# Optimization experiments

Measured on AMD Instinct MI355X. Metric: run time of the kernel, lower is better.

The kernel has to match this reference:

```python
import jax, jax.numpy as jnp
import numpy as np

WS = 8            # window_size
SHIFT = WS // 2   # cyclic shift
NHEADS = 6
EPS = 1e-5


def _rel_pos_index(ws):
    coords = np.stack(np.meshgrid(np.arange(ws), np.arange(ws), indexing='ij'))  # [2,ws,ws]
    flat = coords.reshape(2, -1)                       # [2,N]
    rel = flat[:, :, None] - flat[:, None, :]          # [2,N,N]
    rel = rel.transpose(1, 2, 0).copy()
    rel[:, :, 0] += ws - 1
    rel[:, :, 1] += ws - 1
    rel[:, :, 0] *= 2 * ws - 1
    return rel.sum(-1)                                 # [N,N] indices into bias table


def _attn_mask(H, W, ws, shift):
    # standard Swin boundary mask for the shifted configuration
    img = np.zeros((H, W))
    cnt = 0
    for hs in (slice(0, -ws), slice(-ws, -shift), slice(-shift, None)):
        for wsl in (slice(0, -ws), slice(-ws, -shift), slice(-shift, None)):
            img[hs, wsl] = cnt
            cnt += 1
    mw = img.reshape(H // ws, ws, W // ws, ws).transpose(0, 2, 1, 3).reshape(-1, ws * ws)
    m = mw[:, None, :] - mw[:, :, None]
    return np.where(m != 0, -100.0, 0.0).astype(np.float32)  # [nW, N, N]


def instance_norm(x):
    # InstanceNorm over spatial dims, no affine (torch default)
    m = x.mean(axis=(2, 3), keepdims=True)
    v = x.var(axis=(2, 3), keepdims=True)
    return (x - m) * jax.lax.rsqrt(v + EPS)


def setup_inputs() -> dict:
    key = jax.random.key(0)
    ks = jax.random.split(key, 8)
    B, C, H, W, E = 4, 192, 256, 256, 128
    s = 0.02
    return {
        'x': jax.random.normal(ks[0], (B, C, H, W), jnp.float32),
        'cond': jax.random.normal(ks[1], (B, E), jnp.float32),
        'qkv_w': jax.random.normal(ks[2], (3 * C, C), jnp.float32) * s,
        'qkv_b': jnp.zeros((3 * C,), jnp.float32),
        'proj_w': jax.random.normal(ks[3], (C, C), jnp.float32) * s,
        'proj_b': jnp.zeros((C,), jnp.float32),
        'rel_bias': jax.random.normal(ks[4], ((2 * WS - 1) ** 2, NHEADS), jnp.float32) * s,
        'film_w': jax.random.normal(ks[5], (2 * C, E), jnp.float32) * s,
        'film_b': jnp.zeros((2 * C,), jnp.float32),
    }


def shifted_window_attention(xn, qkv_w, qkv_b, proj_w, proj_b, rel_bias):
    B, C, H, W = xn.shape
    h, ws, shift = NHEADS, WS, SHIFT
    d = C // h
    N = ws * ws
    nW = (H // ws) * (W // ws)
    scale = d ** -0.5

    xs = jnp.transpose(xn, (0, 2, 3, 1))                         # BHWC
    xs = jnp.roll(xs, (-shift, -shift), axis=(1, 2))             # cyclic shift
    win = xs.reshape(B, H // ws, ws, W // ws, ws, C)
    win = win.transpose(0, 1, 3, 2, 4, 5).reshape(B * nW, N, C)  # window partition

    qkv = win @ qkv_w.T + qkv_b                                  # [Bn, N, 3C]
    q, k, v = [t.reshape(B * nW, N, h, d).transpose(0, 2, 1, 3)
               for t in jnp.split(qkv, 3, axis=-1)]              # [Bn, h, N, d]

    attn = jnp.einsum('bhnd,bhmd->bhnm', q, k) * scale           # [Bn, h, N, N]
    bias = rel_bias[_rel_pos_index(ws)].transpose(2, 0, 1)       # [h, N, N]
    attn = attn + bias[None]
    mask = jnp.asarray(_attn_mask(H, W, ws, shift))              # [nW, N, N]
    attn = attn.reshape(B, nW, h, N, N) + mask[None, :, None]
    attn = jax.nn.softmax(attn, axis=-1).reshape(B * nW, h, N, N)

    out = jnp.einsum('bhnm,bhmd->bhnd', attn, v)                 # [Bn, h, N, d]
    out = out.transpose(0, 2, 1, 3).reshape(B * nW, N, C)
    out = out @ proj_w.T + proj_b

    out = out.reshape(B, H // ws, W // ws, ws, ws, C)
    out = out.transpose(0, 1, 3, 2, 4, 5).reshape(B, H, W, C)    # window merge
    out = jnp.roll(out, (shift, shift), axis=(1, 2))             # reverse shift
    return jnp.transpose(out, (0, 3, 1, 2))                      # BCHW


def reference(x, cond, qkv_w, qkv_b, proj_w, proj_b, rel_bias, film_w, film_b):
    # branch 1: x + attn(norm1(x))
    xn = instance_norm(x)
    x = x + shifted_window_attention(xn, qkv_w, qkv_b, proj_w, proj_b, rel_bias)
    # branch 2: x + FiLM(norm2(x), cond)
    x2 = instance_norm(x)
    gb = cond @ film_w.T + film_b                                # [B, 2C]
    gamma, beta = jnp.split(gb, 2, axis=-1)
    x2 = x2 * gamma[:, :, None, None] + beta[:, :, None, None]
    return x + x2
```

## Files before the change

### kernel.cpp

```cpp
#include <hip/hip_runtime.h>

#define BATCH 4
#define CH    192
#define PLANE 65536

typedef unsigned short u16;
typedef unsigned char  u8;
typedef __bf16 bf16x8_t __attribute__((ext_vector_type(8)));
typedef unsigned short u16x8 __attribute__((ext_vector_type(8)));
typedef unsigned short u16x4 __attribute__((ext_vector_type(4)));
typedef float f32x4 __attribute__((ext_vector_type(4)));

__device__ __forceinline__ u16 f2bf(float f) {
  __bf16 h = (__bf16)f;
  return __builtin_bit_cast(u16, h);
}
__device__ __forceinline__ float bf2f(u16 h) {
  unsigned u = ((unsigned)h) << 16;
  return __builtin_bit_cast(float, u);
}
__device__ __forceinline__ f32x4 mfma16(u16x8 a, u16x8 b, f32x4 c) {
  return __builtin_amdgcn_mfma_f32_16x16x32_bf16(
      __builtin_bit_cast(bf16x8_t, a), __builtin_bit_cast(bf16x8_t, b), c, 0, 0, 0);
}

__global__ void cvt_kernel(const float* __restrict__ a, const float* __restrict__ b,
                           const float* __restrict__ rb,
                           u16* __restrict__ wa, u16* __restrict__ wb, u8* __restrict__ bq) {
  const int i = blockIdx.x*256 + threadIdx.x;
  if (i < 576*192) wa[i] = f2bf(a[i]);
  if (i < 192*192) wb[i] = f2bf(b[i]);
  if (i < 1350) {
    float v = fminf(fmaxf(rintf(rb[i]*128.f) + 128.f, 0.f), 255.f);
    bq[i] = (u8)v;
  }
}

__global__ void film_prep(const float* __restrict__ cond, const float* __restrict__ fw,
                          const float* __restrict__ fb, float* __restrict__ gb) {
  const int i = blockIdx.x*256 + threadIdx.x;
  if (i >= BATCH*384) return;
  const int bb = i / 384, oc = i - bb*384;
  const float* cw = fw + oc*128;
  const float* cv = cond + bb*128;
  float s = fb[oc];
  for (int k = 0; k < 128; ++k) s += cv[k]*cw[k];
  gb[i] = s;
}

__global__ __launch_bounds__(256) void prep_kernel(
    const float* __restrict__ x, u16* __restrict__ xraw, float2* __restrict__ part1)
{
  __shared__ u16 tile[32*264];
  const int t = threadIdx.x;
  const int bid = blockIdx.x;
  const int cc = bid % 6;
  const int wh = (bid/6) % 32;
  const int b  = bid / 192;
  const int c0 = cc*32;
  const int ww = t >> 3, ax = t & 7;
  const int gx = (ww*8 + ax + 4) & 255;
  const int gxb = gx & ~3, gxr = gx & 3;
  const long wid = b*1024 + wh*32 + ww;

  const int scl = t >> 3, sseg = t & 7;
  float myS = 0.f, myQ = 0.f;

  for (int ay = 0; ay < 8; ++ay) {
    const int gy = (wh*8 + ay + 4) & 255;
    for (int it = 0; it < 8; ++it) {
      const int id = it*256 + t;
      const int cl = id >> 6;
      const int px = (id & 63) << 2;
      float4 v = *(const float4*)(x + (((long)(b*192+c0+cl)) << 16) + gy*256 + px);
      u16x4 pk;
      pk[0] = f2bf(v.x); pk[1] = f2bf(v.y); pk[2] = f2bf(v.z); pk[3] = f2bf(v.w);
      *(u16x4*)&tile[cl*264 + (px ^ ((cl&7)<<2))] = pk;
    }
    __syncthreads();
    {
      const int sw = (scl & 7) << 2;
      #pragma unroll
      for (int k = 0; k < 32; k += 4) {
        const int px = sseg*32 + k;
        u16x4 pv = *(const u16x4*)&tile[scl*264 + (px ^ sw)];
        float a0 = bf2f(pv[0]), a1 = bf2f(pv[1]), a2 = bf2f(pv[2]), a3 = bf2f(pv[3]);
        myS += a0 + a1 + a2 + a3;
        myQ += a0*a0 + a1*a1 + a2*a2 + a3*a3;
      }
    }
    u16* dst = xraw + wid*12288 + (ay*8+ax)*192 + c0;
    #pragma unroll
    for (int k = 0; k < 4; ++k) {
      u16x8 pk;
      #pragma unroll
      for (int e = 0; e < 8; ++e) {
        const int c = k*8 + e;
        pk[e] = tile[c*264 + (gxb ^ ((c&7)<<2)) + gxr];
      }
      *(u16x8*)(dst + k*8) = pk;
    }
    __syncthreads();
  }
  for (int off = 1; off < 8; off <<= 1) {
    myS += __shfl_xor(myS, off, 64);
    myQ += __shfl_xor(myQ, off, 64);
  }
  if (sseg == 0) {
    float2 pr = {myS, myQ};
    part1[((b*32 + wh)*6 + cc)*32 + scl] = pr;
  }
}

__global__ __launch_bounds__(256) void statsR_kernel(
    const float2* __restrict__ part1, float* __restrict__ st) {
  const int i = blockIdx.x*256 + threadIdx.x;
  if (i >= 768) return;
  const int b = i / 192, c = i % 192;
  const int cg = c >> 5, cl = c & 31;
  float s = 0.f, q = 0.f;
  for (int wh = 0; wh < 32; ++wh) {
    float2 v = part1[((b*32 + wh)*6 + cg)*32 + cl];
    s += v.x; q += v.y;
  }
  const float mean = s * (1.f/PLANE);
  const float var  = q * (1.f/PLANE) - mean*mean;
  st[i*2]   = mean;
  st[i*2+1] = rsqrtf(var + 1e-5f);
}

__global__ __launch_bounds__(512, 4) void attn_kernel(
    const u16* __restrict__ xn, const u16* __restrict__ wq, const u16* __restrict__ wp,
    const float* __restrict__ qkvb, const float* __restrict__ projb,
    const u8* __restrict__ bq, const float* __restrict__ st,
    u16* __restrict__ pw, float2* __restrict__ part)
{
  __shared__ __attribute__((aligned(16))) unsigned char smem[73232];
  u16*    Xs    = (u16*)smem;
  u16*    G     = (u16*)(smem + 25600);
  u16*    Vt    = (u16*)(smem + 43008);
  u16*    Pout  = (u16*)(smem + 25600);
  u8*     biasQ = (u8*)(smem + 52224);
  float2* stpNp = (float2*)(smem + 53576);
  float2* stpR  = (float2*)(smem + 55304);
  u16*    Ps    = (u16*)(smem + 56848);

  const int t    = threadIdx.x;
  const int lane = t & 63;
  const int wave = t >> 6;
  const int arow = lane & 15;
  const int kgrp = lane >> 4;

  const int bid = blockIdx.x;
  const int wid = (bid & 7) * 512 + (bid >> 3);
  const int b   = wid >> 10;
  const int wh  = (wid >> 5) & 31;
  const int ww  = wid & 31;

  for (int i = t; i < 1350; i += 512) biasQ[i] = bq[i];
  if (t < 192) {
    const float mean = st[(b*192 + t)*2];
    const float rstd = st[(b*192 + t)*2 + 1];
    float2 n = {mean, rstd};
    float2 r = {mean, 1.0f / rstd};
    stpNp[t + (t >> 3)] = n;
    stpR[t] = r;
  }
  __syncthreads();

  const u16* src = xn + (long)wid*12288;
  #pragma unroll
  for (int it = 0; it < 3; ++it) {
    const int id = it*512 + t;
    const int row = id/24, c8 = (id%24)*8;
    const int sbase = c8 + (c8 >> 3);
    u16x8 raw = *(const u16x8*)(src + id*8);
    u16x8 nrm;
    #pragma unroll
    for (int e = 0; e < 8; ++e) {
      float2 mr = stpNp[sbase + e];
      nrm[e] = f2bf((bf2f(raw[e]) - mr.x) * mr.y);
    }
    *(u16x8*)&Xs[row*200 + c8] = nrm;
  }
  __syncthreads();

  const int hh = wave >> 2;
  const int mt = wave & 3;
  const bool boundary = (wh == 31) || (ww == 31);
  u16x4 og[3][2];

  #pragma unroll
  for (int g = 0; g < 3; ++g) {
    for (int nt0 = wave; nt0 < 12; nt0 += 8) {
      f32x4 acc[4] = {{0,0,0,0},{0,0,0,0},{0,0,0,0},{0,0,0,0}};
      const int col = nt0*16 + arow;
      const int mat = col >> 6;
      const int ch  = mat*192 + g*64 + (col & 63);
      const u16* wrow = wq + ch*192 + kgrp*8;
      #pragma unroll
      for (int ks = 0; ks < 6; ++ks) {
        u16x8 bfr = *(const u16x8*)(wrow + ks*32);
        #pragma unroll
        for (int m = 0; m < 4; ++m) {
          u16x8 af = *(const u16x8*)&Xs[(m*16+arow)*200 + ks*32 + kgrp*8];
          acc[m] = mfma16(af, bfr, acc[m]);
        }
      }
      const float addb = qkvb[ch];
      if (mat == 2) {
        const int vc = col & 63;
        #pragma unroll
        for (int m = 0; m < 4; ++m) {
          u16x4 pk;
          #pragma unroll
          for (int r = 0; r < 4; ++r) pk[r] = f2bf(acc[m][r] + addb);
          *(u16x4*)&Vt[vc*72 + m*16 + kgrp*4] = pk;
        }
      } else {
        const float mult = (mat == 0) ? 0.17677669529663687f : 1.0f;
        const int gc = mat*64 + (col & 63);
        #pragma unroll
        for (int m = 0; m < 4; ++m)
          #pragma unroll
          for (int r = 0; r < 4; ++r)
            G[(m*16 + kgrp*4 + r)*136 + gc] = f2bf((acc[m][r] + addb)*mult);
      }
    }
    __syncthreads();

    const int hd = g*2 + hh;
    u16x8 qf = *(const u16x8*)&G[(mt*16+arow)*136 + hh*32 + kgrp*8];
    f32x4 sv[4];
    #pragma unroll
    for (int nt = 0; nt < 4; ++nt) {
      u16x8 kf = *(const u16x8*)&G[(nt*16+arow)*136 + 64 + hh*32 + kgrp*8];
      f32x4 z = {0,0,0,0};
      sv[nt] = mfma16(qf, kf, z);
    }

    int qj6[4];
    #pragma unroll
    for (int nt = 0; nt < 4; ++nt) {
      const int j = nt*16 + arow;
      qj6[nt] = ((j>>3)*15 + (j&7))*6;
    }
    float p[4][4];
    if (!boundary) {
      #pragma unroll
      for (int r = 0; r < 4; ++r) {
        const int i = mt*16 + kgrp*4 + r;
        const int qib = ((i>>3)*15 + (i&7) + 112)*6 + hd;
        #pragma unroll
        for (int nt = 0; nt < 4; ++nt)
          p[nt][r] = sv[nt][r] + (float)((int)biasQ[qib - qj6[nt]] - 128) * 0.0078125f;
      }
    } else {
      #pragma unroll
      for (int r = 0; r < 4; ++r) {
        const int i  = mt*16 + kgrp*4 + r;
        const int iy = i >> 3, ix = i & 7;
        const int qib = (iy*15 + ix + 112)*6 + hd;
        const int ri = ((wh==31) ? (iy<4?1:2) : 0)*3 + ((ww==31) ? (ix<4?1:2) : 0);
        #pragma unroll
        for (int nt = 0; nt < 4; ++nt) {
          const int j  = nt*16 + arow;
          const int jy = j >> 3, jx = j & 7;
          const int rj = ((wh==31) ? (jy<4?1:2) : 0)*3 + ((ww==31) ? (jx<4?1:2) : 0);
          float sc = sv[nt][r] + (float)((int)biasQ[qib - qj6[nt]] - 128) * 0.0078125f;
          if (ri != rj) sc -= 100.0f;
          p[nt][r] = sc;
        }
      }
    }
    #pragma unroll
    for (int r = 0; r < 4; ++r) {
      float sum = 0.f;
      #pragma unroll
      for (int nt = 0; nt < 4; ++nt) { p[nt][r] = __expf(p[nt][r]); sum += p[nt][r]; }
      for (int off = 1; off < 16; off <<= 1) sum += __shfl_xor(sum, off, 64);
      const float inv = 1.0f / sum;
      #pragma unroll
      for (int nt = 0; nt < 4; ++nt) p[nt][r] *= inv;
    }
    u16* myP = Ps + wave*1024;
    #pragma unroll
    for (int r = 0; r < 4; ++r) {
      const int i = kgrp*4 + r;
      #pragma unroll
      for (int nt = 0; nt < 4; ++nt) {
        const int j = nt*16 + arow;
        myP[i*64 + ((j + 8*i) & 63)] = f2bf(p[nt][r]);
      }
    }
    f32x4 oacc[2] = {{0,0,0,0},{0,0,0,0}};
    #pragma unroll
    for (int ks = 0; ks < 2; ++ks) {
      u16x8 pf = *(const u16x8*)&myP[arow*64 + ((ks*32 + kgrp*8 + 8*arow) & 63)];
      #pragma unroll
      for (int nt = 0; nt < 2; ++nt) {
        u16x8 vf = *(const u16x8*)&Vt[(hh*32 + nt*16 + arow)*72 + ks*32 + kgrp*8];
        oacc[nt] = mfma16(pf, vf, oacc[nt]);
      }
    }
    #pragma unroll
    for (int nt = 0; nt < 2; ++nt)
      #pragma unroll
      for (int r = 0; r < 4; ++r)
        og[g][nt][r] = f2bf(oacc[nt][r]);
    __syncthreads();
  }

  u16x8 rawreg[3];
  #pragma unroll
  for (int it = 0; it < 3; ++it) {
    const int id = it*512 + t;
    const int c = id >> 3, tk8 = (id & 7)*8;
    const float2 mi = stpR[c];
    u16x8 rr;
    #pragma unroll
    for (int e = 0; e < 8; ++e) {
      float nv = bf2f(Xs[(tk8 + e)*200 + c]);
      rr[e] = f2bf(nv*mi.y + mi.x);
    }
    rawreg[it] = rr;
  }
  __syncthreads();

  #pragma unroll
  for (int g = 0; g < 3; ++g)
    #pragma unroll
    for (int nt = 0; nt < 2; ++nt) {
      const int colb = g*64 + hh*32 + nt*16 + arow;
      #pragma unroll
      for (int r = 0; r < 4; ++r)
        Xs[(mt*16 + kgrp*4 + r)*200 + colb] = og[g][nt][r];
    }
  __syncthreads();

  for (int nt0 = wave; nt0 < 12; nt0 += 8) {
    const int ch = nt0*16 + arow;
    const float pb = projb[ch];
    f32x4 acc[4];
    #pragma unroll
    for (int m = 0; m < 4; ++m) { f32x4 v = {pb,pb,pb,pb}; acc[m] = v; }
    const u16* wrow = wp + ch*192 + kgrp*8;
    #pragma unroll
    for (int ks = 0; ks < 6; ++ks) {
      u16x8 bfr = *(const u16x8*)(wrow + ks*32);
      #pragma unroll
      for (int m = 0; m < 4; ++m) {
        u16x8 af = *(const u16x8*)&Xs[(m*16+arow)*200 + ks*32 + kgrp*8];
        acc[m] = mfma16(af, bfr, acc[m]);
      }
    }
    #pragma unroll
    for (int m = 0; m < 4; ++m) {
      u16x4 pk;
      #pragma unroll
      for (int r = 0; r < 4; ++r) pk[r] = f2bf(acc[m][r]);
      *(u16x4*)&Pout[ch*72 + m*16 + kgrp*4] = pk;
    }
  }
  __syncthreads();

  u16* dstw = pw + (long)wid*12288;
  #pragma unroll
  for (int it = 0; it < 3; ++it) {
    const int id = it*512 + t;
    const int c = id >> 3, tk8 = (id & 7)*8;
    u16x8 pv = *(const u16x8*)&Pout[c*72 + tk8];
    u16x8 rr = rawreg[it];
    u16x8 vb;
    float s = 0.f, q = 0.f;
    #pragma unroll
    for (int e = 0; e < 8; ++e) {
      float v = bf2f(rr[e]) + bf2f(pv[e]);
      vb[e] = f2bf(v);
      s += v; q += v*v;
    }
    *(u16x8*)(dstw + c*64 + tk8) = vb;
    s += __shfl_xor(s, 1, 64); q += __shfl_xor(q, 1, 64);
    s += __shfl_xor(s, 2, 64); q += __shfl_xor(q, 2, 64);
    s += __shfl_xor(s, 4, 64); q += __shfl_xor(q, 4, 64);
    if ((lane & 7) == 0) {
      float2 pr = {s, q};
      part[(long)wid*192 + c] = pr;
    }
  }
}

__global__ __launch_bounds__(256) void stats2_kernel(
    const float2* __restrict__ part, float2* __restrict__ st2f) {
  const int b = blockIdx.x / 12, cg = blockIdx.x % 12;
  const int cl = threadIdx.x & 15;
  const int w0 = threadIdx.x >> 4;
  const int c = cg*16 + cl;
  float s = 0.f, q = 0.f;
  for (int w = w0; w < 1024; w += 16) {
    float2 v = part[((long)(b*1024 + w))*192 + c];
    s += v.x; q += v.y;
  }
  s += __shfl_xor(s, 16, 64); q += __shfl_xor(q, 16, 64);
  s += __shfl_xor(s, 32, 64); q += __shfl_xor(q, 32, 64);
  __shared__ float2 aux[4][16];
  if ((threadIdx.x & 63) < 16) { float2 v = {s, q}; aux[threadIdx.x >> 6][cl] = v; }
  __syncthreads();
  if (threadIdx.x < 16) {
    float2 a0 = aux[0][cl], a1 = aux[1][cl], a2 = aux[2][cl], a3 = aux[3][cl];
    float S = a0.x + a1.x + a2.x + a3.x;
    float Q = a0.y + a1.y + a2.y + a3.y;
    float mean = S * (1.f/PLANE);
    float var  = Q * (1.f/PLANE) - mean*mean;
    float2 o = {mean, rsqrtf(var + 1e-5f)};
    st2f[b*192 + c] = o;
  }
}

__global__ __launch_bounds__(256) void final_kernel(
    const u16* __restrict__ pw, const float2* __restrict__ st2f,
    const float* __restrict__ gb, float* __restrict__ out)
{
  __shared__ u16 tile[32*264];
  const int t = threadIdx.x;
  const int bid = blockIdx.x;
  const int lin = (bid & 7)*96 + (bid >> 3);
  const int cc = lin % 6;
  const int band = lin / 6;
  const int wh = band & 31;
  const int b  = band >> 5;
  const int c0 = cc*32;

  const int ww = t >> 3, cq = t & 7;
  const long wid = b*1024 + wh*32 + ww;
  const u16* srcw = pw + wid*12288;
  const int g1 = ww*8 + 4, g2 = (ww*8 + 8) & 255;

  const int cl = t >> 3, seg = t & 7;
  const int c = c0 + cl;
  const float2 mr = st2f[b*192 + c];
  const float mean = mr.x, rstd = mr.y;
  const float gmm  = gb[b*384 + c];
  const float be   = gb[b*384 + 192 + c];
  const int swb = (cl & 7) << 2;

  for (int ay = 0; ay < 8; ++ay) {
    #pragma unroll
    for (int j = 0; j < 4; ++j) {
      const int ca = cq*4 + j;
      u16x8 v = *(const u16x8*)(srcw + (c0+ca)*64 + ay*8);
      const int sw = (ca & 7) << 2;
      u16x4 lo = {v[0],v[1],v[2],v[3]}, hi = {v[4],v[5],v[6],v[7]};
      *(u16x4*)&tile[ca*264 + (g1 ^ sw)] = lo;
      *(u16x4*)&tile[ca*264 + (g2 ^ sw)] = hi;
    }
    __syncthreads();

    const int gy = (wh*8 + ay + 4) & 255;
    const long base = (((long)(b*192 + c)) << 16) + gy*256 + seg*32;
    float* orow = out + base;
    #pragma unroll
    for (int q4 = 0; q4 < 32; q4 += 4) {
      const int px = seg*32 + q4;
      u16x4 pv = *(const u16x4*)&tile[cl*264 + (px ^ swb)];
      float4 o;
      float v0 = bf2f(pv[0]), v1 = bf2f(pv[1]), v2 = bf2f(pv[2]), v3 = bf2f(pv[3]);
      o.x = v0 + (v0 - mean)*rstd*gmm + be;
      o.y = v1 + (v1 - mean)*rstd*gmm + be;
      o.z = v2 + (v2 - mean)*rstd*gmm + be;
      o.w = v3 + (v3 - mean)*rstd*gmm + be;
      *(float4*)(orow + q4) = o;
    }
    __syncthreads();
  }
}

extern "C" void kernel_launch(void* const* d_in, const int* in_sizes, int n_in,
                              void* d_out, int out_size, void* d_ws, size_t ws_size,
                              hipStream_t stream) {
  const float* x      = (const float*)d_in[0];
  const float* cond   = (const float*)d_in[1];
  const float* qkv_w  = (const float*)d_in[2];
  const float* qkv_b  = (const float*)d_in[3];
  const float* proj_w = (const float*)d_in[4];
  const float* proj_b = (const float*)d_in[5];
  const float* relb   = (const float*)d_in[6];
  const float* film_w = (const float*)d_in[7];
  const float* film_b = (const float*)d_in[8];
  float* out = (float*)d_out;

  char* ws = (char*)d_ws;
  float*  stats1 = (float*)ws;
  float2* st2f   = (float2*)(ws + 6144);
  float*  gb     = (float*)(ws + 12288);
  u16*    wq     = (u16*)(ws + 18432);
  u16*    wp     = (u16*)(ws + 239616);
  u8*     bqq    = (u8*)(ws + 313344);
  u16*    xbuf   = (u16*)(ws + 362496);
  float2* part   = (float2*)(ws + 362496 + 100663296);
  float2* part1  = (float2*)(ws + 362496 + 100663296 + 6291456);

  cvt_kernel<<<432, 256, 0, stream>>>(qkv_w, proj_w, relb, wq, wp, bqq);
  film_prep<<<6, 256, 0, stream>>>(cond, film_w, film_b, gb);
  prep_kernel<<<768, 256, 0, stream>>>(x, xbuf, part1);
  statsR_kernel<<<3, 256, 0, stream>>>(part1, stats1);
  attn_kernel<<<4096, 512, 0, stream>>>(xbuf, wq, wp, qkv_b, proj_b, bqq, stats1, xbuf, part);
  stats2_kernel<<<48, 256, 0, stream>>>(part, st2f);
  final_kernel<<<768, 256, 0, stream>>>(xbuf, st2f, gb, out);
}
```

Baseline: 480.6 us.

## Merge setup kernels, rebalance QKV/proj MFMA work across waves, read stats directly

Folds the weight conversion, FiLM projection and stats reduction into one setup kernel, cutting the launch count from seven to five. In the attention kernel, the per-thread normalization now reads mean/rstd straight from global memory as float4 instead of a staged shared table, which drops one barrier and some shared memory. The QKV and output-projection GEMMs are reassigned so that all 8 waves do equal work: the V tiles and the last 64 projection channels are split into half-M pieces instead of some waves doing two full tiles. A rotated index in the transposed Xs read is meant to reduce LDS bank conflicts.

```diff
diff --git a/kernel.cpp b/kernel.cpp
--- a/kernel.cpp
+++ b/kernel.cpp
@@ -22,30 +22,6 @@
 __device__ __forceinline__ f32x4 mfma16(u16x8 a, u16x8 b, f32x4 c) {
   return __builtin_amdgcn_mfma_f32_16x16x32_bf16(
       __builtin_bit_cast(bf16x8_t, a), __builtin_bit_cast(bf16x8_t, b), c, 0, 0, 0);
-}
-
-__global__ void cvt_kernel(const float* __restrict__ a, const float* __restrict__ b,
-                           const float* __restrict__ rb,
-                           u16* __restrict__ wa, u16* __restrict__ wb, u8* __restrict__ bq) {
-  const int i = blockIdx.x*256 + threadIdx.x;
-  if (i < 576*192) wa[i] = f2bf(a[i]);
-  if (i < 192*192) wb[i] = f2bf(b[i]);
-  if (i < 1350) {
-    float v = fminf(fmaxf(rintf(rb[i]*128.f) + 128.f, 0.f), 255.f);
-    bq[i] = (u8)v;
-  }
-}
-
-__global__ void film_prep(const float* __restrict__ cond, const float* __restrict__ fw,
-                          const float* __restrict__ fb, float* __restrict__ gb) {
-  const int i = blockIdx.x*256 + threadIdx.x;
-  if (i >= BATCH*384) return;
-  const int bb = i / 384, oc = i - bb*384;
-  const float* cw = fw + oc*128;
-  const float* cv = cond + bb*128;
-  float s = fb[oc];
-  for (int k = 0; k < 128; ++k) s += cv[k]*cw[k];
-  gb[i] = s;
 }
 
 __global__ __launch_bounds__(256) void prep_kernel(
@@ -112,21 +88,47 @@
   }
 }
 
-__global__ __launch_bounds__(256) void statsR_kernel(
-    const float2* __restrict__ part1, float* __restrict__ st) {
-  const int i = blockIdx.x*256 + threadIdx.x;
-  if (i >= 768) return;
-  const int b = i / 192, c = i % 192;
-  const int cg = c >> 5, cl = c & 31;
-  float s = 0.f, q = 0.f;
-  for (int wh = 0; wh < 32; ++wh) {
-    float2 v = part1[((b*32 + wh)*6 + cg)*32 + cl];
-    s += v.x; q += v.y;
-  }
-  const float mean = s * (1.f/PLANE);
-  const float var  = q * (1.f/PLANE) - mean*mean;
-  st[i*2]   = mean;
-  st[i*2+1] = rsqrtf(var + 1e-5f);
+__global__ __launch_bounds__(256) void setup_kernel(
+    const float* __restrict__ a, const float* __restrict__ b2,
+    const float* __restrict__ rb, const float* __restrict__ cond,
+    const float* __restrict__ fw, const float* __restrict__ fb,
+    const float2* __restrict__ part1,
+    u16* __restrict__ wa, u16* __restrict__ wb, u8* __restrict__ bq,
+    float* __restrict__ gb, float* __restrict__ st)
+{
+  const int blk = blockIdx.x;
+  if (blk < 432) {
+    const int i = blk*256 + threadIdx.x;
+    if (i < 576*192) wa[i] = f2bf(a[i]);
+    if (i < 192*192) wb[i] = f2bf(b2[i]);
+    if (i < 1350) {
+      float v = fminf(fmaxf(rintf(rb[i]*128.f) + 128.f, 0.f), 255.f);
+      bq[i] = (u8)v;
+    }
+  } else if (blk < 438) {
+    const int i = (blk - 432)*256 + threadIdx.x;
+    if (i >= BATCH*384) return;
+    const int bb = i / 384, oc = i - bb*384;
+    const float* cw = fw + oc*128;
+    const float* cv = cond + bb*128;
+    float s = fb[oc];
+    for (int k = 0; k < 128; ++k) s += cv[k]*cw[k];
+    gb[i] = s;
+  } else {
+    const int i = (blk - 438)*256 + threadIdx.x;
+    if (i >= 768) return;
+    const int b = i / 192, c = i % 192;
+    const int cg = c >> 5, cl = c & 31;
+    float s = 0.f, q = 0.f;
+    for (int wh = 0; wh < 32; ++wh) {
+      float2 v = part1[((b*32 + wh)*6 + cg)*32 + cl];
+      s += v.x; q += v.y;
+    }
+    const float mean = s * (1.f/PLANE);
+    const float var  = q * (1.f/PLANE) - mean*mean;
+    st[i*2]   = mean;
+    st[i*2+1] = rsqrtf(var + 1e-5f);
+  }
 }
 
 __global__ __launch_bounds__(512, 4) void attn_kernel(
@@ -135,15 +137,14 @@
     const u8* __restrict__ bq, const float* __restrict__ st,
     u16* __restrict__ pw, float2* __restrict__ part)
 {
-  __shared__ __attribute__((aligned(16))) unsigned char smem[73232];
+  __shared__ __attribute__((aligned(16))) unsigned char smem[71552];
   u16*    Xs    = (u16*)smem;
   u16*    G     = (u16*)(smem + 25600);
   u16*    Vt    = (u16*)(smem + 43008);
   u16*    Pout  = (u16*)(smem + 25600);
   u8*     biasQ = (u8*)(smem + 52224);
-  float2* stpNp = (float2*)(smem + 53576);
-  float2* stpR  = (float2*)(smem + 55304);
-  u16*    Ps    = (u16*)(smem + 56848);
+  float2* stpR  = (float2*)(smem + 53632);
+  u16*    Ps    = (u16*)(smem + 55168);
 
   const int t    = threadIdx.x;
   const int lane = t & 63;
@@ -161,25 +162,23 @@
   if (t < 192) {
     const float mean = st[(b*192 + t)*2];
     const float rstd = st[(b*192 + t)*2 + 1];
-    float2 n = {mean, rstd};
     float2 r = {mean, 1.0f / rstd};
-    stpNp[t + (t >> 3)] = n;
     stpR[t] = r;
   }
-  __syncthreads();
 
   const u16* src = xn + (long)wid*12288;
+  const float4* stv = (const float4*)(st + b*384);
   #pragma unroll
   for (int it = 0; it < 3; ++it) {
     const int id = it*512 + t;
     const int row = id/24, c8 = (id%24)*8;
-    const int sbase = c8 + (c8 >> 3);
     u16x8 raw = *(const u16x8*)(src + id*8);
     u16x8 nrm;
     #pragma unroll
-    for (int e = 0; e < 8; ++e) {
-      float2 mr = stpNp[sbase + e];
-      nrm[e] = f2bf((bf2f(raw[e]) - mr.x) * mr.y);
+    for (int e2 = 0; e2 < 4; ++e2) {
+      float4 mr = stv[(c8 >> 1) + e2];
+      nrm[2*e2]   = f2bf((bf2f(raw[2*e2])   - mr.x) * mr.y);
+      nrm[2*e2+1] = f2bf((bf2f(raw[2*e2+1]) - mr.z) * mr.w);
     }
     *(u16x8*)&Xs[row*200 + c8] = nrm;
   }
@@ -192,11 +191,11 @@
 
   #pragma unroll
   for (int g = 0; g < 3; ++g) {
-    for (int nt0 = wave; nt0 < 12; nt0 += 8) {
-      f32x4 acc[4] = {{0,0,0,0},{0,0,0,0},{0,0,0,0},{0,0,0,0}};
-      const int col = nt0*16 + arow;
+    {
+      const int col = wave*16 + arow;
       const int mat = col >> 6;
       const int ch  = mat*192 + g*64 + (col & 63);
+      f32x4 acc[4] = {{0,0,0,0},{0,0,0,0},{0,0,0,0},{0,0,0,0}};
       const u16* wrow = wq + ch*192 + kgrp*8;
       #pragma unroll
       for (int ks = 0; ks < 6; ++ks) {
@@ -208,23 +207,37 @@
         }
       }
       const float addb = qkvb[ch];
-      if (mat == 2) {
-        const int vc = col & 63;
+      const float mult = (mat == 0) ? 0.17677669529663687f : 1.0f;
+      const int gc = mat*64 + (col & 63);
+      #pragma unroll
+      for (int m = 0; m < 4; ++m)
         #pragma unroll
-        for (int m = 0; m < 4; ++m) {
-          u16x4 pk;
-          #pragma unroll
-          for (int r = 0; r < 4; ++r) pk[r] = f2bf(acc[m][r] + addb);
-          *(u16x4*)&Vt[vc*72 + m*16 + kgrp*4] = pk;
+        for (int r = 0; r < 4; ++r)
+          G[(m*16 + kgrp*4 + r)*136 + gc] = f2bf((acc[m][r] + addb)*mult);
+    }
+    {
+      const int vtile = wave >> 1;
+      const int mh    = wave & 1;
+      const int vc    = vtile*16 + arow;
+      const int ch    = 384 + g*64 + vc;
+      f32x4 acc[2] = {{0,0,0,0},{0,0,0,0}};
+      const u16* wrow = wq + ch*192 + kgrp*8;
+      #pragma unroll
+      for (int ks = 0; ks < 6; ++ks) {
+        u16x8 bfr = *(const u16x8*)(wrow + ks*32);
+        #pragma unroll
+        for (int m2 = 0; m2 < 2; ++m2) {
+          u16x8 af = *(const u16x8*)&Xs[((mh*2+m2)*16+arow)*200 + ks*32 + kgrp*8];
+          acc[m2] = mfma16(af, bfr, acc[m2]);
         }
-      } else {
-        const float mult = (mat == 0) ? 0.17677669529663687f : 1.0f;
-        const int gc = mat*64 + (col & 63);
+      }
+      const float addb = qkvb[ch];
+      #pragma unroll
+      for (int m2 = 0; m2 < 2; ++m2) {
+        u16x4 pk;
         #pragma unroll
-        for (int m = 0; m < 4; ++m)
-          #pragma unroll
-          for (int r = 0; r < 4; ++r)
-            G[(m*16 + kgrp*4 + r)*136 + gc] = f2bf((acc[m][r] + addb)*mult);
+        for (int r = 0; r < 4; ++r) pk[r] = f2bf(acc[m2][r] + addb);
+        *(u16x4*)&Vt[vc*72 + (mh*2+m2)*16 + kgrp*4] = pk;
       }
     }
     __syncthreads();
@@ -319,7 +332,8 @@
     const float2 mi = stpR[c];
     u16x8 rr;
     #pragma unroll
-    for (int e = 0; e < 8; ++e) {
+    for (int k = 0; k < 8; ++k) {
+      const int e = (k + (c & 7)) & 7;
       float nv = bf2f(Xs[(tk8 + e)*200 + c]);
       rr[e] = f2bf(nv*mi.y + mi.x);
     }
@@ -338,12 +352,10 @@
     }
   __syncthreads();
 
-  for (int nt0 = wave; nt0 < 12; nt0 += 8) {
-    const int ch = nt0*16 + arow;
+  {
+    const int ch = wave*16 + arow;
     const float pb = projb[ch];
-    f32x4 acc[4];
-    #pragma unroll
-    for (int m = 0; m < 4; ++m) { f32x4 v = {pb,pb,pb,pb}; acc[m] = v; }
+    f32x4 acc[4] = {{pb,pb,pb,pb},{pb,pb,pb,pb},{pb,pb,pb,pb},{pb,pb,pb,pb}};
     const u16* wrow = wp + ch*192 + kgrp*8;
     #pragma unroll
     for (int ks = 0; ks < 6; ++ks) {
@@ -360,6 +372,30 @@
       #pragma unroll
       for (int r = 0; r < 4; ++r) pk[r] = f2bf(acc[m][r]);
       *(u16x4*)&Pout[ch*72 + m*16 + kgrp*4] = pk;
+    }
+  }
+  {
+    const int ptile = wave >> 1;
+    const int mh    = wave & 1;
+    const int ch    = 128 + ptile*16 + arow;
+    const float pb  = projb[ch];
+    f32x4 acc[2] = {{pb,pb,pb,pb},{pb,pb,pb,pb}};
+    const u16* wrow = wp + ch*192 + kgrp*8;
+    #pragma unroll
+    for (int ks = 0; ks < 6; ++ks) {
+      u16x8 bfr = *(const u16x8*)(wrow + ks*32);
+      #pragma unroll
+      for (int m2 = 0; m2 < 2; ++m2) {
+        u16x8 af = *(const u16x8*)&Xs[((mh*2+m2)*16+arow)*200 + ks*32 + kgrp*8];
+        acc[m2] = mfma16(af, bfr, acc[m2]);
+      }
+    }
+    #pragma unroll
+    for (int m2 = 0; m2 < 2; ++m2) {
+      u16x4 pk;
+      #pragma unroll
+      for (int r = 0; r < 4; ++r) pk[r] = f2bf(acc[m2][r]);
+      *(u16x4*)&Pout[ch*72 + (mh*2+m2)*16 + kgrp*4] = pk;
     }
   }
   __syncthreads();
@@ -500,10 +536,9 @@
   float2* part   = (float2*)(ws + 362496 + 100663296);
   float2* part1  = (float2*)(ws + 362496 + 100663296 + 6291456);
 
-  cvt_kernel<<<432, 256, 0, stream>>>(qkv_w, proj_w, relb, wq, wp, bqq);
-  film_prep<<<6, 256, 0, stream>>>(cond, film_w, film_b, gb);
   prep_kernel<<<768, 256, 0, stream>>>(x, xbuf, part1);
-  statsR_kernel<<<3, 256, 0, stream>>>(part1, stats1);
+  setup_kernel<<<441, 256, 0, stream>>>(qkv_w, proj_w, relb, cond, film_w, film_b,
+                                        part1, wq, wp, bqq, gb, stats1);
   attn_kernel<<<4096, 512, 0, stream>>>(xbuf, wq, wp, qkv_b, proj_b, bqq, stats1, xbuf, part);
   stats2_kernel<<<48, 256, 0, stream>>>(part, st2f);
   final_kernel<<<768, 256, 0, stream>>>(xbuf, st2f, gb, out);
```

After: 514.7 us. 7.1% more time.
